# Performance work log

Measured on AMD Instinct MI355X. Metric: run time of the kernel, lower is better.

## Reference

```python
import jax, jax.numpy as jnp
import numpy as np

VX, VY = 0.16, 0.16
PC = (0.0, -39.68, -3.0, 69.12, 39.68, 1.0)
X_OFFSET = VX / 2 + PC[0]
Y_OFFSET = VY / 2 + PC[1]
X_L = int((PC[3] - PC[0]) / VX)   # 432
Y_L = int((PC[4] - PC[1]) / VY)   # 496
C = 64
BN_EPS = 1e-3
LN_EPS = 1e-5


def setup_inputs() -> dict:
    key = jax.random.key(0)
    ks = jax.random.split(key, 16)
    B, PPB, M = 4, 10000, 32
    P = B * PPB
    # unique (x,y) pillar coords per batch, sorted by batch index (matches per-batch loop order)
    rng = np.random.default_rng(0)
    coords = []
    for i in range(B):
        lin = rng.choice(X_L * Y_L, PPB, replace=False)
        coords.append(np.stack([np.full(PPB, i), lin // Y_L, lin % Y_L], axis=1))
    coors_batch = jnp.asarray(np.concatenate(coords, axis=0), dtype=jnp.int32)
    npoints_per_pillar = jax.random.randint(ks[0], (P,), 1, M + 1, dtype=jnp.int32)
    lo = jnp.array([0.5, -39.68, -3.0, 0.0], jnp.float32)
    hi = jnp.array([69.12, 39.68, 1.0, 1.0], jnp.float32)
    pts = lo + jax.random.uniform(ks[1], (P, M, 4), dtype=jnp.float32) * (hi - lo)
    valid = (jnp.arange(M)[None, :] < npoints_per_pillar[:, None])[:, :, None]
    pillars = pts * valid  # zero-padded beyond npoints, as real voxelizers produce
    H_IMG, W_IMG = 192, 640  # half-resolution image feature map
    batch_image_map = jax.random.normal(ks[2], (B, C, H_IMG, W_IMG), dtype=jnp.float32)
    # pinhole-style 3x4 projection with forward-x as depth: u=(cx*x - fx*y)/x, v=(cy*x - fy*z)/x
    fx, fy, cx, cy = 700.0, 700.0, 640.0, 192.0
    calib = jnp.array([[cx, -fx, 0.0, 0.0], [cy, 0.0, -fy, 0.0], [1.0, 0.0, 0.0, 0.0]], jnp.float32)
    batched_calibs = jnp.tile(calib[None], (B, 1, 1)) * (1.0 + 0.01 * jax.random.normal(ks[3], (B, 3, 4)))
    conv_w = 0.1 * jax.random.normal(ks[4], (C, 9), dtype=jnp.float32)
    bn_gamma = 1.0 + 0.1 * jax.random.normal(ks[5], (C,), dtype=jnp.float32)
    bn_beta = 0.1 * jax.random.normal(ks[6], (C,), dtype=jnp.float32)
    bn_mean = 0.1 * jax.random.normal(ks[7], (C,), dtype=jnp.float32)
    bn_var = jax.random.uniform(ks[8], (C,), minval=0.5, maxval=1.5, dtype=jnp.float32)
    g_w1 = 0.1 * jax.random.normal(ks[9], (2 * C, 2 * C), dtype=jnp.float32)
    g_b1 = 0.1 * jax.random.normal(ks[10], (2 * C,), dtype=jnp.float32)
    ln_gamma = 1.0 + 0.1 * jax.random.normal(ks[11], (2 * C,), dtype=jnp.float32)
    ln_beta = 0.1 * jax.random.normal(ks[12], (2 * C,), dtype=jnp.float32)
    g_w2 = 0.1 * jax.random.normal(ks[13], (C, 2 * C), dtype=jnp.float32)
    g_b2 = 0.1 * jax.random.normal(ks[14], (C,), dtype=jnp.float32)
    return dict(pillars=pillars, coors_batch=coors_batch, npoints_per_pillar=npoints_per_pillar,
                batch_image_map=batch_image_map, batched_calibs=batched_calibs, batch_size=B,
                conv_w=conv_w, bn_gamma=bn_gamma, bn_beta=bn_beta, bn_mean=bn_mean, bn_var=bn_var,
                g_w1=g_w1, g_b1=g_b1, ln_gamma=ln_gamma, ln_beta=ln_beta, g_w2=g_w2, g_b2=g_b2)


def reference(pillars, coors_batch, npoints_per_pillar, batch_image_map, batched_calibs, batch_size,
              conv_w, bn_gamma, bn_beta, bn_mean, bn_var, g_w1, g_b1, ln_gamma, ln_beta, g_w2, g_b2):
    P, M, _ = pillars.shape
    npts = npoints_per_pillar.astype(pillars.dtype)
    mean_center = jnp.sum(pillars[:, :, :3], axis=1, keepdims=True) / npts[:, None, None]  # [P,1,3]
    offset_pt_center = pillars[:, :, :3] - mean_center
    cx = coors_batch[:, None, 1:2].astype(pillars.dtype) * VX + X_OFFSET
    cy = coors_batch[:, None, 2:3].astype(pillars.dtype) * VY + Y_OFFSET
    x_off = pillars[:, :, 0:1] - cx
    y_off = pillars[:, :, 1:2] - cy
    # channels 0,1 of the original concat are overwritten with x_off,y_off in-place
    features = jnp.concatenate([x_off, y_off, pillars[:, :, 2:], offset_pt_center, x_off, y_off], axis=-1)  # [P,M,9]
    mask = jnp.arange(M)[None, :] < npoints_per_pillar[:, None]
    features = features * mask[:, :, None]
    # Conv1d(k=1, no bias) + BatchNorm1d(eval) + ReLU (double ReLU in source collapses to one)
    h = jnp.einsum('pmi,ci->pmc', features, conv_w)
    h = (h - bn_mean) * (bn_gamma / jnp.sqrt(bn_var + BN_EPS)) + bn_beta
    h = jax.nn.relu(h)
    pooling_features = jnp.max(h, axis=1)  # [P,C]
    # vectorized image-feature gather (coors sorted by batch idx, so order matches the per-batch loop)
    bidx = coors_batch[:, 0]
    ctr = mean_center[:, 0, :]  # [P,3]
    hom = jnp.concatenate([ctr, jnp.ones((P, 1), ctr.dtype)], axis=-1)  # [P,4]
    proj = jnp.einsum('pij,pj->pi', batched_calibs[bidx], hom)
    depth = proj[:, 2]
    u = proj[:, 0] / depth
    v = proj[:, 1] / depth
    h_img, w_img = batch_image_map.shape[2], batch_image_map.shape[3]
    u = jnp.clip(u / 2, 0, w_img - 1).astype(jnp.int32)
    v = jnp.clip(v / 2, 0, h_img - 1).astype(jnp.int32)
    image_features = batch_image_map.transpose(0, 2, 3, 1)[bidx, v, u]  # [P,C]
    # gated fusion
    cat = jnp.concatenate([pooling_features, image_features], axis=1)  # [P,2C]
    g = cat @ g_w1.T + g_b1
    mu = jnp.mean(g, axis=-1, keepdims=True)
    var = jnp.var(g, axis=-1, keepdims=True)
    g = (g - mu) / jnp.sqrt(var + LN_EPS) * ln_gamma + ln_beta
    g = jax.nn.relu(g)
    gate = jax.nn.sigmoid(g @ g_w2.T + g_b2)  # [P,C]
    gate_features = pooling_features * gate + image_features * (1.0 - gate)
    # scatter to dense BEV canvas [B, x_l, y_l, C] then permute to [B, C, y_l, x_l]
    canvas = jnp.zeros((batch_size, X_L, Y_L, C), dtype=jnp.float32)
    canvas = canvas.at[bidx, coors_batch[:, 1], coors_batch[:, 2]].set(gate_features)
    return canvas.transpose(0, 3, 2, 1)
```

## Files before the change

### kernel.cpp

```cpp
#include <hip/hip_runtime.h>
#include <cfloat>
#include <cmath>

#define XL 432
#define YL 496
#define NCH 64
#define HIMG 192
#define WIMG 640
#define PTS_M 32

#define WAVES 8
#define PPG 4
#define NBLOCKS 256
#define TPB 512

__global__ __launch_bounds__(TPB, 1) void pillar_fused(
    const float* __restrict__ pillars,
    const int*   __restrict__ coors,
    const int*   __restrict__ npp,
    const float* __restrict__ image,
    const float* __restrict__ calibs,
    const float* __restrict__ conv_w,
    const float* __restrict__ bng, const float* __restrict__ bnb,
    const float* __restrict__ bnm, const float* __restrict__ bnv,
    const float* __restrict__ w1, const float* __restrict__ b1,
    const float* __restrict__ lng, const float* __restrict__ lnb,
    const float* __restrict__ w2, const float* __restrict__ b2,
    float* __restrict__ out, int P)
{
    __shared__ float w1t[128 * 128];
    __shared__ float w2t[128 * 64];
    __shared__ float catL[WAVES][PPG][128];
    __shared__ float gL[WAVES][PPG][128];

    const int tid = threadIdx.x;
    const int lane = tid & 63;
    const int wv = tid >> 6;

    for (int i = tid; i < 128 * 128; i += TPB) {
        const int j = i >> 7, k = i & 127;
        w1t[k * 128 + j] = w1[i];
    }
    for (int i = tid; i < 128 * 64; i += TPB) {
        const int c = i >> 7, k = i & 127;
        w2t[k * 64 + c] = w2[i];
    }
    __syncthreads();

    float cw[9];
    #pragma unroll
    for (int i = 0; i < 9; ++i) cw[i] = conv_w[lane * 9 + i];
    const float s   = bng[lane] / sqrtf(bnv[lane] + 1e-3f);
    const float tch = bnb[lane] - bnm[lane] * s;
    const float As = (cw[0] + cw[4] + cw[7]) * s;
    const float Bs = (cw[1] + cw[5] + cw[8]) * s;
    const float Cs = (cw[2] + cw[6]) * s;
    const float Ds = cw[3] * s;
    const float w07 = (cw[0] + cw[7]) * s;
    const float w18 = (cw[1] + cw[8]) * s;
    const float w4s = cw[4] * s, w5s = cw[5] * s, w6s = cw[6] * s;

    const float b1a = b1[lane], b1b = b1[lane + 64];
    const float lga = lng[lane], lgb = lng[lane + 64];
    const float lba = lnb[lane], lbb = lnb[lane + 64];
    const float gb2 = b2[lane];

    const int ngroups = (P + PPG - 1) / PPG;
    const int gstride = gridDim.x * WAVES;

    for (int grp = blockIdx.x * WAVES + wv; grp < ngroups; grp += gstride) {
        const int pbase = grp * PPG;

        #pragma unroll
        for (int pp = 0; pp < PPG; ++pp) {
            const int p = pbase + pp;
            if (p >= P) {
                catL[wv][pp][lane] = 0.f;
                catL[wv][pp][lane + 64] = 0.f;
                continue;
            }
            const int bb = coors[p * 3];
            const int n = npp[p];
            const float fn = (float)n;

            float4 pt = make_float4(0.f, 0.f, 0.f, 0.f);
            if (lane < PTS_M) pt = ((const float4*)pillars)[p * PTS_M + lane];
            float sx = pt.x, sy = pt.y, sz = pt.z;
            #pragma unroll
            for (int d = 32; d; d >>= 1) {
                sx += __shfl_xor(sx, d);
                sy += __shfl_xor(sy, d);
                sz += __shfl_xor(sz, d);
            }
            const float mx = sx / fn, my = sy / fn, mz = sz / fn;

            const float* cb = calibs + bb * 12;
            const float pr0 = cb[0]*mx + cb[1]*my + cb[2]*mz + cb[3];
            const float pr1 = cb[4]*mx + cb[5]*my + cb[6]*mz + cb[7];
            const float pr2 = cb[8]*mx + cb[9]*my + cb[10]*mz + cb[11];
            float uf = (pr0 / pr2) * 0.5f;
            float vf = (pr1 / pr2) * 0.5f;
            uf = fminf(fmaxf(uf, 0.f), (float)(WIMG - 1));
            vf = fminf(fmaxf(vf, 0.f), (float)(HIMG - 1));
            const int u = (int)uf, v = (int)vf;

            const float cxp = (float)coors[p * 3 + 1] * 0.16f + 0.08f;
            const float cyp = (float)coors[p * 3 + 2] * 0.16f + (-39.6f);
            const float Es = tch - (cxp * w07 + cyp * w18 + mx * w4s + my * w5s + mz * w6s);

            float pooled = (n < PTS_M) ? tch : -FLT_MAX;
            const float4* pb = (const float4*)pillars + p * PTS_M;
            for (int m = 0; m < n; ++m) {
                const float4 q = pb[m];
                const float h = Es + q.x * As + q.y * Bs + q.z * Cs + q.w * Ds;
                pooled = fmaxf(pooled, h);
            }
            pooled = fmaxf(pooled, 0.f);

            const float img = image[(((bb * NCH) + lane) * HIMG + v) * WIMG + u];
            catL[wv][pp][lane] = pooled;
            catL[wv][pp][lane + 64] = img;
        }
        asm volatile("s_waitcnt lgkmcnt(0)" ::: "memory");

        float accA[PPG], accB[PPG];
        #pragma unroll
        for (int pp = 0; pp < PPG; ++pp) { accA[pp] = b1a; accB[pp] = b1b; }

        #pragma unroll 4
        for (int k = 0; k < 128; ++k) {
            const float wa = w1t[k * 128 + lane];
            const float wb = w1t[k * 128 + lane + 64];
            #pragma unroll
            for (int pp = 0; pp < PPG; ++pp) {
                const float cv = catL[wv][pp][k];
                accA[pp] += cv * wa;
                accB[pp] += cv * wb;
            }
        }

        float sum[PPG], sq[PPG];
        #pragma unroll
        for (int pp = 0; pp < PPG; ++pp) {
            sum[pp] = accA[pp] + accB[pp];
            sq[pp]  = accA[pp] * accA[pp] + accB[pp] * accB[pp];
        }
        #pragma unroll
        for (int d = 32; d; d >>= 1) {
            #pragma unroll
            for (int pp = 0; pp < PPG; ++pp) {
                sum[pp] += __shfl_xor(sum[pp], d);
                sq[pp]  += __shfl_xor(sq[pp], d);
            }
        }
        #pragma unroll
        for (int pp = 0; pp < PPG; ++pp) {
            const float mu  = sum[pp] * (1.f / 128.f);
            const float var = sq[pp] * (1.f / 128.f) - mu * mu;
            const float inv = 1.f / sqrtf(var + 1e-5f);
            float g0 = (accA[pp] - mu) * inv * lga + lba;
            float g1 = (accB[pp] - mu) * inv * lgb + lbb;
            gL[wv][pp][lane]      = fmaxf(g0, 0.f);
            gL[wv][pp][lane + 64] = fmaxf(g1, 0.f);
        }
        asm volatile("s_waitcnt lgkmcnt(0)" ::: "memory");

        float ac2[PPG];
        #pragma unroll
        for (int pp = 0; pp < PPG; ++pp) ac2[pp] = gb2;
        #pragma unroll 4
        for (int k = 0; k < 128; ++k) {
            const float w = w2t[k * 64 + lane];
            #pragma unroll
            for (int pp = 0; pp < PPG; ++pp) ac2[pp] += gL[wv][pp][k] * w;
        }

        #pragma unroll
        for (int pp = 0; pp < PPG; ++pp) {
            const int p = pbase + pp;
            if (p >= P) continue;
            const float gate = 1.f / (1.f + expf(-ac2[pp]));
            const float pooled = catL[wv][pp][lane];
            const float img    = catL[wv][pp][lane + 64];
            const float gf = pooled * gate + img * (1.f - gate);
            const int bb  = coors[p * 3];
            const int ixx = coors[p * 3 + 1];
            const int iyy = coors[p * 3 + 2];
            out[(((bb * NCH) + lane) * YL + iyy) * XL + ixx] = gf;
        }
    }
}

extern "C" void kernel_launch(void* const* d_in, const int* in_sizes, int n_in,
                              void* d_out, int out_size, void* d_ws, size_t ws_size,
                              hipStream_t stream)
{
    const float* pillars = (const float*)d_in[0];
    const int*   coors   = (const int*)d_in[1];
    const int*   npp     = (const int*)d_in[2];
    const float* image   = (const float*)d_in[3];
    const float* calibs  = (const float*)d_in[4];
    const float* conv_w  = (const float*)d_in[6];
    const float* bng     = (const float*)d_in[7];
    const float* bnb     = (const float*)d_in[8];
    const float* bnm     = (const float*)d_in[9];
    const float* bnv     = (const float*)d_in[10];
    const float* w1      = (const float*)d_in[11];
    const float* b1      = (const float*)d_in[12];
    const float* lng     = (const float*)d_in[13];
    const float* lnb     = (const float*)d_in[14];
    const float* w2      = (const float*)d_in[15];
    const float* b2      = (const float*)d_in[16];
    float* out = (float*)d_out;
    const int P = in_sizes[0] / (PTS_M * 4);

    hipMemsetAsync(d_out, 0, (size_t)out_size * sizeof(float), stream);
    pillar_fused<<<dim3(NBLOCKS), dim3(TPB), 0, stream>>>(
        pillars, coors, npp, image, calibs, conv_w, bng, bnb, bnm, bnv,
        w1, b1, lng, lnb, w2, b2, out, P);
}
```

Before: 207.0 us.

## Stage pillars into LDS asynchronously, batch per-pillar work, add dynamic work stealing

The kernel now copies each group's four pillars straight into per-wave LDS with global_load_lds and computes the centroid sums with half-wave reductions, instead of issuing a serial global load per point. The weight matrices are stored row-major with a padded pitch and read as float4 for the two GEMVs. The max-pool loop is fully unrolled with predication, waves per block go from 8 to 16, and an atomic counter in the workspace hands out pillar groups dynamically. The aim is to cut global-load latency and imbalance from variable point counts, at the cost of higher LDS use per block and an atomic per task.

```diff
diff --git a/kernel.cpp b/kernel.cpp
--- a/kernel.cpp
+++ b/kernel.cpp
@@ -9,12 +9,24 @@
 #define WIMG 640
 #define PTS_M 32
 
-#define WAVES 8
+#define WAVES 16
+#define TPB (WAVES * 64)
 #define PPG 4
 #define NBLOCKS 256
-#define TPB 512
-
-__global__ __launch_bounds__(TPB, 1) void pillar_fused(
+#define WPITCH 132
+
+typedef const __attribute__((address_space(1))) void* gas_t;
+typedef __attribute__((address_space(3))) void* las_t;
+
+__device__ __forceinline__ void gload_lds16(const float* g, float* l) {
+    __builtin_amdgcn_global_load_lds((gas_t)g, (las_t)l, 16, 0, 0);
+}
+
+#define RED5(v) { v += __shfl_xor(v, 16); v += __shfl_xor(v, 8); v += __shfl_xor(v, 4); \
+                  v += __shfl_xor(v, 2);  v += __shfl_xor(v, 1); }
+
+template<bool ATOMIC>
+__global__ __launch_bounds__(TPB, 4) void pillar_fused(
     const float* __restrict__ pillars,
     const int*   __restrict__ coors,
     const int*   __restrict__ npp,
@@ -26,24 +38,23 @@
     const float* __restrict__ w1, const float* __restrict__ b1,
     const float* __restrict__ lng, const float* __restrict__ lnb,
     const float* __restrict__ w2, const float* __restrict__ b2,
-    float* __restrict__ out, int P)
+    float* __restrict__ out, int P, int* __restrict__ cnt)
 {
-    __shared__ float w1t[128 * 128];
-    __shared__ float w2t[128 * 64];
-    __shared__ float catL[WAVES][PPG][128];
-    __shared__ float gL[WAVES][PPG][128];
-
-    const int tid = threadIdx.x;
+    __shared__ float w1p[128 * WPITCH];
+    __shared__ float w2p[64 * WPITCH];
+    __shared__ float ws[WAVES][512];
+
+    const int tid  = threadIdx.x;
     const int lane = tid & 63;
-    const int wv = tid >> 6;
-
-    for (int i = tid; i < 128 * 128; i += TPB) {
-        const int j = i >> 7, k = i & 127;
-        w1t[k * 128 + j] = w1[i];
+    const int wv   = tid >> 6;
+
+    for (int i = tid; i < 128 * 32; i += TPB) {
+        const int j = i >> 5, k4 = i & 31;
+        ((float4*)(w1p + j * WPITCH))[k4] = ((const float4*)w1)[i];
     }
-    for (int i = tid; i < 128 * 64; i += TPB) {
-        const int c = i >> 7, k = i & 127;
-        w2t[k * 64 + c] = w2[i];
+    for (int i = tid; i < 64 * 32; i += TPB) {
+        const int j = i >> 5, k4 = i & 31;
+        ((float4*)(w2p + j * WPITCH))[k4] = ((const float4*)w2)[i];
     }
     __syncthreads();
 
@@ -52,10 +63,10 @@
     for (int i = 0; i < 9; ++i) cw[i] = conv_w[lane * 9 + i];
     const float s   = bng[lane] / sqrtf(bnv[lane] + 1e-3f);
     const float tch = bnb[lane] - bnm[lane] * s;
-    const float As = (cw[0] + cw[4] + cw[7]) * s;
-    const float Bs = (cw[1] + cw[5] + cw[8]) * s;
-    const float Cs = (cw[2] + cw[6]) * s;
-    const float Ds = cw[3] * s;
+    const float As  = (cw[0] + cw[4] + cw[7]) * s;
+    const float Bs  = (cw[1] + cw[5] + cw[8]) * s;
+    const float Cs  = (cw[2] + cw[6]) * s;
+    const float Ds  = cw[3] * s;
     const float w07 = (cw[0] + cw[7]) * s;
     const float w18 = (cw[1] + cw[8]) * s;
     const float w4s = cw[4] * s, w5s = cw[5] * s, w6s = cw[6] * s;
@@ -65,77 +76,142 @@
     const float lba = lnb[lane], lbb = lnb[lane + 64];
     const float gb2 = b2[lane];
 
-    const int ngroups = (P + PPG - 1) / PPG;
-    const int gstride = gridDim.x * WAVES;
-
-    for (int grp = blockIdx.x * WAVES + wv; grp < ngroups; grp += gstride) {
+    float* wsw = ws[wv];
+    const float4* wsf4 = (const float4*)wsw;
+    const float4* w1rA = (const float4*)(w1p + lane * WPITCH);
+    const float4* w1rB = (const float4*)(w1p + (lane + 64) * WPITCH);
+    const float4* w2r  = (const float4*)(w2p + lane * WPITCH);
+
+    const int ntasks = (P + PPG - 1) / PPG;
+    int nextStatic = blockIdx.x * WAVES + wv;
+
+    for (;;) {
+        int grp;
+        if (ATOMIC) {
+            int g0 = 0;
+            if (lane == 0) g0 = atomicAdd(cnt, 1);
+            grp = __shfl(g0, 0);
+        } else {
+            grp = nextStatic;
+            nextStatic += gridDim.x * WAVES;
+        }
+        if (grp >= ntasks) break;
+
         const int pbase = grp * PPG;
-
+        const bool full = (pbase + PPG <= P);
+
+        asm volatile("s_waitcnt lgkmcnt(0)" ::: "memory");
+        if (full) {
+            const float* src = pillars + (size_t)pbase * (PTS_M * 4);
+            gload_lds16(src + lane * 4, wsw);
+            gload_lds16(src + 256 + lane * 4, wsw + 256);
+        } else {
+            #pragma unroll
+            for (int h = 0; h < 2; ++h) {
+                const int idx = pbase * PTS_M + h * 64 + lane;
+                float4 v = make_float4(0.f, 0.f, 0.f, 0.f);
+                if (idx < P * PTS_M) v = ((const float4*)pillars)[idx];
+                ((float4*)wsw)[h * 64 + lane] = v;
+            }
+        }
+
+        int bbv[PPG], ixv[PPG], iyv[PPG], nv[PPG];
         #pragma unroll
         for (int pp = 0; pp < PPG; ++pp) {
             const int p = pbase + pp;
-            if (p >= P) {
-                catL[wv][pp][lane] = 0.f;
-                catL[wv][pp][lane + 64] = 0.f;
-                continue;
-            }
-            const int bb = coors[p * 3];
-            const int n = npp[p];
-            const float fn = (float)n;
-
-            float4 pt = make_float4(0.f, 0.f, 0.f, 0.f);
-            if (lane < PTS_M) pt = ((const float4*)pillars)[p * PTS_M + lane];
-            float sx = pt.x, sy = pt.y, sz = pt.z;
-            #pragma unroll
-            for (int d = 32; d; d >>= 1) {
-                sx += __shfl_xor(sx, d);
-                sy += __shfl_xor(sy, d);
-                sz += __shfl_xor(sz, d);
-            }
-            const float mx = sx / fn, my = sy / fn, mz = sz / fn;
-
-            const float* cb = calibs + bb * 12;
-            const float pr0 = cb[0]*mx + cb[1]*my + cb[2]*mz + cb[3];
-            const float pr1 = cb[4]*mx + cb[5]*my + cb[6]*mz + cb[7];
-            const float pr2 = cb[8]*mx + cb[9]*my + cb[10]*mz + cb[11];
+            if (p < P) {
+                bbv[pp] = coors[p * 3]; ixv[pp] = coors[p * 3 + 1];
+                iyv[pp] = coors[p * 3 + 2]; nv[pp] = npp[p];
+            } else {
+                bbv[pp] = 0; ixv[pp] = 0; iyv[pp] = 0; nv[pp] = 1;
+            }
+        }
+
+        asm volatile("s_waitcnt vmcnt(0) lgkmcnt(0)" ::: "memory");
+
+        const float4 qa = wsf4[lane];
+        const float4 qb = wsf4[64 + lane];
+        float ax = qa.x, ay = qa.y, az = qa.z;
+        float bx = qb.x, by = qb.y, bz = qb.z;
+        RED5(ax) RED5(ay) RED5(az)
+        RED5(bx) RED5(by) RED5(bz)
+        const float axo = __shfl_xor(ax, 32), ayo = __shfl_xor(ay, 32), azo = __shfl_xor(az, 32);
+        const float bxo = __shfl_xor(bx, 32), byo = __shfl_xor(by, 32), bzo = __shfl_xor(bz, 32);
+        const bool lo = lane < 32;
+        float mx[PPG], my[PPG], mz[PPG];
+        {
+            const float f0 = 1.f / (float)nv[0], f1 = 1.f / (float)nv[1];
+            const float f2 = 1.f / (float)nv[2], f3 = 1.f / (float)nv[3];
+            mx[0] = (lo ? ax : axo) * f0;  mx[1] = (lo ? axo : ax) * f1;
+            my[0] = (lo ? ay : ayo) * f0;  my[1] = (lo ? ayo : ay) * f1;
+            mz[0] = (lo ? az : azo) * f0;  mz[1] = (lo ? azo : az) * f1;
+            mx[2] = (lo ? bx : bxo) * f2;  mx[3] = (lo ? bxo : bx) * f3;
+            my[2] = (lo ? by : byo) * f2;  my[3] = (lo ? byo : by) * f3;
+            mz[2] = (lo ? bz : bzo) * f2;  mz[3] = (lo ? bzo : bz) * f3;
+        }
+
+        float img[PPG], Es[PPG];
+        #pragma unroll
+        for (int pp = 0; pp < PPG; ++pp) {
+            const float* cb = calibs + bbv[pp] * 12;
+            const float pr0 = cb[0]*mx[pp] + cb[1]*my[pp] + cb[2]*mz[pp] + cb[3];
+            const float pr1 = cb[4]*mx[pp] + cb[5]*my[pp] + cb[6]*mz[pp] + cb[7];
+            const float pr2 = cb[8]*mx[pp] + cb[9]*my[pp] + cb[10]*mz[pp] + cb[11];
             float uf = (pr0 / pr2) * 0.5f;
             float vf = (pr1 / pr2) * 0.5f;
             uf = fminf(fmaxf(uf, 0.f), (float)(WIMG - 1));
             vf = fminf(fmaxf(vf, 0.f), (float)(HIMG - 1));
             const int u = (int)uf, v = (int)vf;
-
-            const float cxp = (float)coors[p * 3 + 1] * 0.16f + 0.08f;
-            const float cyp = (float)coors[p * 3 + 2] * 0.16f + (-39.6f);
-            const float Es = tch - (cxp * w07 + cyp * w18 + mx * w4s + my * w5s + mz * w6s);
-
-            float pooled = (n < PTS_M) ? tch : -FLT_MAX;
-            const float4* pb = (const float4*)pillars + p * PTS_M;
-            for (int m = 0; m < n; ++m) {
-                const float4 q = pb[m];
-                const float h = Es + q.x * As + q.y * Bs + q.z * Cs + q.w * Ds;
-                pooled = fmaxf(pooled, h);
-            }
-            pooled = fmaxf(pooled, 0.f);
-
-            const float img = image[(((bb * NCH) + lane) * HIMG + v) * WIMG + u];
-            catL[wv][pp][lane] = pooled;
-            catL[wv][pp][lane + 64] = img;
+            img[pp] = image[(((bbv[pp] * NCH) + lane) * HIMG + v) * WIMG + u];
+
+            const float cxp = (float)ixv[pp] * 0.16f + 0.08f;
+            const float cyp = (float)iyv[pp] * 0.16f + (-39.6f);
+            Es[pp] = tch - (cxp * w07 + cyp * w18 + mx[pp] * w4s + my[pp] * w5s + mz[pp] * w6s);
+        }
+
+        float pooled[PPG];
+        #pragma unroll
+        for (int pp = 0; pp < PPG; ++pp) {
+            const int n = nv[pp];
+            float p0 = (n < PTS_M) ? tch : -FLT_MAX;
+            float p1 = -FLT_MAX, p2 = -FLT_MAX, p3 = -FLT_MAX;
+            #pragma unroll
+            for (int m = 0; m < PTS_M; m += 4) {
+                const float4 q0 = wsf4[pp * 32 + m];
+                const float4 q1 = wsf4[pp * 32 + m + 1];
+                const float4 q2 = wsf4[pp * 32 + m + 2];
+                const float4 q3 = wsf4[pp * 32 + m + 3];
+                const float h0 = Es[pp] + q0.x*As + q0.y*Bs + q0.z*Cs + q0.w*Ds;
+                const float h1 = Es[pp] + q1.x*As + q1.y*Bs + q1.z*Cs + q1.w*Ds;
+                const float h2 = Es[pp] + q2.x*As + q2.y*Bs + q2.z*Cs + q2.w*Ds;
+                const float h3 = Es[pp] + q3.x*As + q3.y*Bs + q3.z*Cs + q3.w*Ds;
+                p0 = fmaxf(p0, (m     < n) ? h0 : -FLT_MAX);
+                p1 = fmaxf(p1, (m + 1 < n) ? h1 : -FLT_MAX);
+                p2 = fmaxf(p2, (m + 2 < n) ? h2 : -FLT_MAX);
+                p3 = fmaxf(p3, (m + 3 < n) ? h3 : -FLT_MAX);
+            }
+            pooled[pp] = fmaxf(fmaxf(fmaxf(p0, p1), fmaxf(p2, p3)), 0.f);
+        }
+
+        #pragma unroll
+        for (int pp = 0; pp < PPG; ++pp) {
+            wsw[pp * 128 + lane]      = pooled[pp];
+            wsw[pp * 128 + 64 + lane] = img[pp];
         }
         asm volatile("s_waitcnt lgkmcnt(0)" ::: "memory");
 
         float accA[PPG], accB[PPG];
         #pragma unroll
         for (int pp = 0; pp < PPG; ++pp) { accA[pp] = b1a; accB[pp] = b1b; }
-
         #pragma unroll 4
-        for (int k = 0; k < 128; ++k) {
-            const float wa = w1t[k * 128 + lane];
-            const float wb = w1t[k * 128 + lane + 64];
+        for (int k4 = 0; k4 < 32; ++k4) {
+            const float4 wa = w1rA[k4];
+            const float4 wb = w1rB[k4];
             #pragma unroll
             for (int pp = 0; pp < PPG; ++pp) {
-                const float cv = catL[wv][pp][k];
-                accA[pp] += cv * wa;
-                accB[pp] += cv * wb;
+                const float4 cv = wsf4[pp * 32 + k4];
+                accA[pp] += cv.x*wa.x + cv.y*wa.y + cv.z*wa.z + cv.w*wa.w;
+                accB[pp] += cv.x*wb.x + cv.y*wb.y + cv.z*wb.z + cv.w*wb.w;
             }
         }
 
@@ -143,7 +219,7 @@
         #pragma unroll
         for (int pp = 0; pp < PPG; ++pp) {
             sum[pp] = accA[pp] + accB[pp];
-            sq[pp]  = accA[pp] * accA[pp] + accB[pp] * accB[pp];
+            sq[pp]  = accA[pp]*accA[pp] + accB[pp]*accB[pp];
         }
         #pragma unroll
         for (int d = 32; d; d >>= 1) {
@@ -158,10 +234,10 @@
             const float mu  = sum[pp] * (1.f / 128.f);
             const float var = sq[pp] * (1.f / 128.f) - mu * mu;
             const float inv = 1.f / sqrtf(var + 1e-5f);
-            float g0 = (accA[pp] - mu) * inv * lga + lba;
-            float g1 = (accB[pp] - mu) * inv * lgb + lbb;
-            gL[wv][pp][lane]      = fmaxf(g0, 0.f);
-            gL[wv][pp][lane + 64] = fmaxf(g1, 0.f);
+            const float g0 = (accA[pp] - mu) * inv * lga + lba;
+            const float g1 = (accB[pp] - mu) * inv * lgb + lbb;
+            wsw[pp * 128 + lane]      = fmaxf(g0, 0.f);
+            wsw[pp * 128 + 64 + lane] = fmaxf(g1, 0.f);
         }
         asm volatile("s_waitcnt lgkmcnt(0)" ::: "memory");
 
@@ -169,24 +245,21 @@
         #pragma unroll
         for (int pp = 0; pp < PPG; ++pp) ac2[pp] = gb2;
         #pragma unroll 4
-        for (int k = 0; k < 128; ++k) {
-            const float w = w2t[k * 64 + lane];
-            #pragma unroll
-            for (int pp = 0; pp < PPG; ++pp) ac2[pp] += gL[wv][pp][k] * w;
-        }
-
+        for (int k4 = 0; k4 < 32; ++k4) {
+            const float4 w = w2r[k4];
+            #pragma unroll
+            for (int pp = 0; pp < PPG; ++pp) {
+                const float4 gv = wsf4[pp * 32 + k4];
+                ac2[pp] += gv.x*w.x + gv.y*w.y + gv.z*w.z + gv.w*w.w;
+            }
+        }
         #pragma unroll
         for (int pp = 0; pp < PPG; ++pp) {
             const int p = pbase + pp;
             if (p >= P) continue;
             const float gate = 1.f / (1.f + expf(-ac2[pp]));
-            const float pooled = catL[wv][pp][lane];
-            const float img    = catL[wv][pp][lane + 64];
-            const float gf = pooled * gate + img * (1.f - gate);
-            const int bb  = coors[p * 3];
-            const int ixx = coors[p * 3 + 1];
-            const int iyy = coors[p * 3 + 2];
-            out[(((bb * NCH) + lane) * YL + iyy) * XL + ixx] = gf;
+            const float gf = pooled[pp] * gate + img[pp] * (1.f - gate);
+            out[(((bbv[pp] * NCH) + lane) * YL + iyv[pp]) * XL + ixv[pp]] = gf;
         }
     }
 }
@@ -215,7 +288,14 @@
     const int P = in_sizes[0] / (PTS_M * 4);
 
     hipMemsetAsync(d_out, 0, (size_t)out_size * sizeof(float), stream);
-    pillar_fused<<<dim3(NBLOCKS), dim3(TPB), 0, stream>>>(
-        pillars, coors, npp, image, calibs, conv_w, bng, bnb, bnm, bnv,
-        w1, b1, lng, lnb, w2, b2, out, P);
+    if (ws_size >= 4) {
+        hipMemsetAsync(d_ws, 0, 4, stream);
+        pillar_fused<true><<<dim3(NBLOCKS), dim3(TPB), 0, stream>>>(
+            pillars, coors, npp, image, calibs, conv_w, bng, bnb, bnm, bnv,
+            w1, b1, lng, lnb, w2, b2, out, P, (int*)d_ws);
+    } else {
+        pillar_fused<false><<<dim3(NBLOCKS), dim3(TPB), 0, stream>>>(
+            pillars, coors, npp, image, calibs, conv_w, bng, bnb, bnm, bnv,
+            w1, b1, lng, lnb, w2, b2, out, P, nullptr);
+    }
 }
```

New measurement: 224.3 us. 8.3% more time.
